# Optimization experiments

Measured on AMD Instinct MI355X. Metric: run time of the kernel, lower is better.

Reference implementation:

```python
import jax, jax.numpy as jnp
import numpy as np

N_EMBED = 1024
NUM_HEADS = 16
HEAD_SIZE = 64  # NUM_HEADS * HEAD_SIZE == N_EMBED
BLOCK_SIZE = 2048


def setup_inputs() -> dict:
    key = jax.random.key(0)
    ks = jax.random.split(key, 9)
    s = 1.0 / np.sqrt(N_EMBED)
    batch_x = jax.random.normal(ks[0], (4, BLOCK_SIZE, N_EMBED), dtype=jnp.float32)
    # stacked per-head linear params: weight [H, E, d], bias [H, d]
    Wq = jax.random.uniform(ks[1], (NUM_HEADS, N_EMBED, HEAD_SIZE), jnp.float32, -s, s)
    Wk = jax.random.uniform(ks[2], (NUM_HEADS, N_EMBED, HEAD_SIZE), jnp.float32, -s, s)
    Wv = jax.random.uniform(ks[3], (NUM_HEADS, N_EMBED, HEAD_SIZE), jnp.float32, -s, s)
    bq = jax.random.uniform(ks[4], (NUM_HEADS, HEAD_SIZE), jnp.float32, -s, s)
    bk = jax.random.uniform(ks[5], (NUM_HEADS, HEAD_SIZE), jnp.float32, -s, s)
    bv = jax.random.uniform(ks[6], (NUM_HEADS, HEAD_SIZE), jnp.float32, -s, s)
    Wp = jax.random.uniform(ks[7], (N_EMBED, N_EMBED), jnp.float32, -s, s)
    bp = jax.random.uniform(ks[8], (N_EMBED,), jnp.float32, -s, s)
    return {"batch_x": batch_x, "Wq": Wq, "Wk": Wk, "Wv": Wv,
            "bq": bq, "bk": bk, "bv": bv, "Wp": Wp, "bp": bp}


def reference(batch_x, Wq, Wk, Wv, bq, bk, bv, Wp, bp):
    B, T, E = batch_x.shape
    # per-head projections: [B, H, T, d]
    q = jnp.einsum('bte,hed->bhtd', batch_x, Wq) + bq[None, :, None, :]
    k = jnp.einsum('bte,hed->bhtd', batch_x, Wk) + bk[None, :, None, :]
    v = jnp.einsum('bte,hed->bhtd', batch_x, Wv) + bv[None, :, None, :]
    scale = 1.0 / jnp.sqrt(jnp.asarray(HEAD_SIZE, batch_x.dtype))
    wei = jnp.einsum('bhtd,bhsd->bhts', q, k) * scale  # [B,H,T,T]
    causal = jnp.tril(jnp.ones((T, T), dtype=bool))
    wei = jnp.where(causal, wei, jnp.asarray(-jnp.inf, wei.dtype))
    wei = jax.nn.softmax(wei, axis=-1)
    out = jnp.einsum('bhts,bhsd->bhtd', wei, v)  # [B,H,T,d]
    # concat heads (head order matches torch.cat over ModuleList)
    out = out.transpose(0, 2, 1, 3).reshape(B, T, NUM_HEADS * HEAD_SIZE)
    return out @ Wp + bp
```

## Files before the change

kernel.cpp:

```cpp
#include <hip/hip_runtime.h>
#include <math.h>

#define B_ 4
#define T_ 2048
#define E_ 1024
#define H_ 16
#define D_ 64

typedef __bf16 bf16_t;
typedef bf16_t bf16x8 __attribute__((ext_vector_type(8)));
typedef float  f32x4  __attribute__((ext_vector_type(4)));
typedef float  f32x16 __attribute__((ext_vector_type(16)));
typedef unsigned short u16x4 __attribute__((ext_vector_type(4)));
typedef unsigned int   u32x4 __attribute__((ext_vector_type(4)));

static __device__ __forceinline__ unsigned short f2bf(float f) {
    bf16_t h = (bf16_t)f;
    return __builtin_bit_cast(unsigned short, h);
}
static __device__ __forceinline__ unsigned int pk2(float a, float b) {
    return (unsigned int)f2bf(a) | ((unsigned int)f2bf(b) << 16);
}
static __device__ __forceinline__ float ex2(float x) {
    float r; asm("v_exp_f32 %0, %1" : "=v"(r) : "v"(x)); return r;
}
static __device__ __forceinline__ void pl32swap(unsigned int& a, unsigned int& b) {
    asm("v_permlane32_swap_b32 %0, %1" : "+v"(a), "+v"(b));
}

#define GLD(gp, lp) __builtin_amdgcn_global_load_lds( \
    (const __attribute__((address_space(1))) unsigned int*)(gp), \
    (__attribute__((address_space(3))) unsigned int*)(lp), 16, 0, 0)

#define BAR() __builtin_amdgcn_s_barrier()
#define WAIT_LGKM0() asm volatile("s_waitcnt lgkmcnt(0)" ::: "memory")
#define VMC(n) asm volatile("s_waitcnt vmcnt(" #n ")" ::: "memory")

__global__ void cast_x_kernel(const float* __restrict__ in, unsigned short* __restrict__ out, int n4) {
    int i = blockIdx.x * blockDim.x + threadIdx.x;
    if (i >= n4) return;
    float4 v = ((const float4*)in)[i];
    ushort4 o;
    o.x = f2bf(v.x); o.y = f2bf(v.y); o.z = f2bf(v.z); o.w = f2bf(v.w);
    ((ushort4*)out)[i] = o;
}

__global__ void tcast_all(const float* __restrict__ Wq, const float* __restrict__ Wk,
                          const float* __restrict__ Wv, const float* __restrict__ Wp,
                          unsigned short* __restrict__ wf, unsigned short* __restrict__ wpt) {
    __shared__ unsigned short Ts[64 * 66];
    const int grp = blockIdx.y >> 4, yy = blockIdx.y & 15;
    const float* in; unsigned short* out; int yA, S;
    if (grp == 3) { in = Wp; out = wpt; yA = 64;    S = 1024; }
    else {
        in = (grp == 0) ? Wq : (grp == 1) ? Wk : Wv;
        out = wf + (size_t)grp * 1024 * 1024; yA = 65536; S = 64;
    }
    const int tid = threadIdx.x;
    const int r = tid >> 2, c4 = tid & 3;
    const float* ip = in + (size_t)yA * yy + (size_t)(blockIdx.x * 64 + r) * S + c4 * 16;
    #pragma unroll
    for (int j = 0; j < 4; ++j) {
        float4 v = *(const float4*)&ip[j * 4];
        Ts[(c4 * 16 + j * 4 + 0) * 66 + r] = f2bf(v.x);
        Ts[(c4 * 16 + j * 4 + 1) * 66 + r] = f2bf(v.y);
        Ts[(c4 * 16 + j * 4 + 2) * 66 + r] = f2bf(v.z);
        Ts[(c4 * 16 + j * 4 + 3) * 66 + r] = f2bf(v.w);
    }
    __syncthreads();
    unsigned short* op = out + (size_t)(yy * 64 + r) * 1024 + blockIdx.x * 64 + c4 * 16;
    #pragma unroll
    for (int j = 0; j < 4; ++j) {
        u16x4 pk;
        #pragma unroll
        for (int m = 0; m < 4; ++m) pk[m] = Ts[r * 66 + c4 * 16 + j * 4 + m];
        *(u16x4*)&op[j * 4] = pk;
    }
}


#define GEMM_CORE_DECLS \
    const int tid = threadIdx.x; \
    const int w = tid >> 6, lane = tid & 63; \
    const int wr = w >> 2, wc = w & 3; \
    const int l15 = lane & 15, quad = lane >> 4, lsw = l15 & 7; \
    const int rowg = lane >> 3; \
    const int swz = ((lane & 7) ^ rowg) * 8; \
    f32x4 acc[4][4]; \
    _Pragma("unroll") for (int i_ = 0; i_ < 4; ++i_) \
        _Pragma("unroll") for (int j_ = 0; j_ < 4; ++j_) \
            acc[i_][j_] = (f32x4){0.f, 0.f, 0.f, 0.f};

#define MFMA_P(nb) \
    __builtin_amdgcn_s_setprio(1); \
    _Pragma("unroll") for (int m_ = 0; m_ < 4; ++m_) \
        _Pragma("unroll") for (int j_ = 0; j_ < 2; ++j_) \
            _Pragma("unroll") for (int k_ = 0; k_ < 2; ++k_) \
                acc[m_][(nb) + j_] = __builtin_amdgcn_mfma_f32_16x16x32_bf16( \
                    fA[m_][k_], fB[(nb) + j_][k_], acc[m_][(nb) + j_], 0, 0, 0); \
    __builtin_amdgcn_s_setprio(0);

#define GEMM_K_LOOP \
    stageA(0, 0); stageA(0, 1); stageB(0, 0, 0); stageB(0, 0, 1); \
    stageB(0, 1, 0); stageB(0, 1, 1); \
    stageA(1, 0); stageA(1, 1); stageB(1, 0, 0); stageB(1, 0, 1); \
    VMC(6); BAR(); \
    _Pragma("unroll 1") \
    for (int it = 0; it < 8; ++it) { \
        const int t0 = 2 * it, t1 = 2 * it + 1; \
        const bool more = it < 7; \
        bf16x8 fA[4][2], fB[4][2]; \
         \
        _Pragma("unroll") for (int m_ = 0; m_ < 4; ++m_) { fA[m_][0] = rdA(t0, m_, 0); fA[m_][1] = rdA(t0, m_, 1); } \
        _Pragma("unroll") for (int n_ = 0; n_ < 2; ++n_) { fB[n_][0] = rdB(t0, n_, 0); fB[n_][1] = rdB(t0, n_, 1); } \
        stageB(t1, 1, 0); stageB(t1, 1, 1); \
        BAR(); WAIT_LGKM0(); \
        MFMA_P(0); \
        VMC(6); BAR(); \
         \
        _Pragma("unroll") for (int n_ = 0; n_ < 2; ++n_) { fB[2 + n_][0] = rdB(t0, 2 + n_, 0); fB[2 + n_][1] = rdB(t0, 2 + n_, 1); } \
        if (more) { stageA(t0 + 2, 0); stageA(t0 + 2, 1); stageB(t0 + 2, 0, 0); stageB(t0 + 2, 0, 1); } \
        BAR(); WAIT_LGKM0(); \
        MFMA_P(2); \
        if (more) { VMC(6); } else { VMC(2); } \
        BAR(); \
         \
        _Pragma("unroll") for (int m_ = 0; m_ < 4; ++m_) { fA[m_][0] = rdA(t1, m_, 0); fA[m_][1] = rdA(t1, m_, 1); } \
        _Pragma("unroll") for (int n_ = 0; n_ < 2; ++n_) { fB[n_][0] = rdB(t1, n_, 0); fB[n_][1] = rdB(t1, n_, 1); } \
        if (more) { stageB(t0 + 2, 1, 0); stageB(t0 + 2, 1, 1); } \
        BAR(); WAIT_LGKM0(); \
        MFMA_P(0); \
        if (more) { VMC(6); } else { VMC(0); } \
        BAR(); \
         \
        _Pragma("unroll") for (int n_ = 0; n_ < 2; ++n_) { fB[2 + n_][0] = rdB(t1, 2 + n_, 0); fB[2 + n_][1] = rdB(t1, 2 + n_, 1); } \
        if (more) { stageA(t1 + 2, 0); stageA(t1 + 2, 1); stageB(t1 + 2, 0, 0); stageB(t1 + 2, 0, 1); } \
        BAR(); WAIT_LGKM0(); \
        MFMA_P(2); \
        if (more) { VMC(6); } \
        BAR(); \
    }

__global__ __launch_bounds__(512, 2) void qkv_gemm(
    const unsigned short* __restrict__ xb,
    const unsigned short* __restrict__ wf,
    const float* __restrict__ bq, const float* __restrict__ bk, const float* __restrict__ bv,
    unsigned short* __restrict__ qo, unsigned short* __restrict__ ko,
    unsigned short* __restrict__ vt)
{
    __shared__ __align__(16) unsigned short sm[49152];

    const int bid = blockIdx.x;
    const int m0 = (bid & 63) * 128;
    const int n0 = (bid >> 6) * 256;

    GEMM_CORE_DECLS

    auto stageA = [&](int t, int g) {
        const int rb = w * 16 + g * 8;
        unsigned short* dst = sm + (t & 1) * 24576 + rb * 64;
        GLD(xb + (size_t)(m0 + rb + rowg) * 1024 + t * 64 + swz, dst);
    };
    auto stageB = [&](int t, int R, int g) {
        const int rb = w * 16 + g * 8;
        const int ar0 = (rb >> 5) * 64 + R * 32 + (rb & 31);
        unsigned short* dst = sm + (t & 1) * 24576 + 8192 + ar0 * 64;
        GLD(wf + (size_t)(n0 + ar0 + rowg) * 1024 + t * 64 + swz, dst);
    };
    auto rdA = [&](int t, int fm, int ks) {
        const int row = wr * 64 + fm * 16 + l15;
        return *(const bf16x8*)&sm[(t & 1) * 24576 + row * 64 + (((ks * 4 + quad) ^ lsw) * 8)];
    };
    auto rdB = [&](int t, int fn, int ks) {
        const int row = wc * 64 + fn * 16 + l15;
        return *(const bf16x8*)&sm[(t & 1) * 24576 + 8192 + row * 64 + (((ks * 4 + quad) ^ lsw) * 8)];
    };

    GEMM_K_LOOP

    const int which = n0 >> 10;
    const int nb = n0 & 1023;
    if (which < 2) {
        const float* bias = which ? bk : bq;
        unsigned short* outp = which ? ko : qo;
        const float sc = which ? 1.f : 0.125f * 1.44269504088896f;
        #pragma unroll
        for (int fm = 0; fm < 4; ++fm)
            #pragma unroll
            for (int fn = 0; fn < 4; ++fn) {
                int colg = nb + wc * 64 + fn * 16 + l15;
                int h = colg >> 6, d = colg & 63;
                float bi = bias[colg];
                #pragma unroll
                for (int r = 0; r < 4; ++r) {
                    int row = m0 + wr * 64 + fm * 16 + quad * 4 + r;
                    int b = row >> 11, t = row & 2047;
                    outp[(((size_t)b * 16 + h) * 2048 + t) * 64 + d] = f2bf((acc[fm][fn][r] + bi) * sc);
                }
            }
    } else {
        const int b = m0 >> 11, t0r = m0 & 2047;
        for (int nh = 0; nh < 2; ++nh) {
            __syncthreads();
            if ((wc >> 1) == nh) {
                const int cc = wc & 1;
                #pragma unroll
                for (int fm = 0; fm < 4; ++fm)
                    #pragma unroll
                    for (int fn = 0; fn < 4; ++fn) {
                        int colL = cc * 64 + fn * 16 + l15;
                        int colg = nb + nh * 128 + colL;
                        float bi = bv[colg];
                        u16x4 pk;
                        #pragma unroll
                        for (int r = 0; r < 4; ++r) pk[r] = f2bf(acc[fm][fn][r] + bi);
                        *(u16x4*)&sm[colL * 136 + wr * 64 + fm * 16 + quad * 4] = pk;
                    }
            }
            __syncthreads();
            const int nl = tid >> 2, tq = tid & 3;
            const int colg = nb + nh * 128 + nl;
            const int h = colg >> 6, d = colg & 63;
            unsigned short* dst = vt + (((size_t)b * 16 + h) * 64 + d) * 2048 + t0r + tq * 32;
            #pragma unroll
            for (int j = 0; j < 4; ++j)
                *(float4*)&dst[j * 8] = *(const float4*)&sm[nl * 136 + tq * 32 + j * 8];
        }
    }
}

__global__ __launch_bounds__(512, 2) void proj_gemm(
    const unsigned short* __restrict__ A,
    const unsigned short* __restrict__ wpt,
    const float* __restrict__ bp,
    float* __restrict__ out)
{
    __shared__ __align__(16) unsigned short sm[49152];

    const int bid = blockIdx.x;
    const int m0 = (bid & 63) * 128;
    const int n0 = (bid >> 6) * 256;

    GEMM_CORE_DECLS

    const unsigned short* Ab = A + (size_t)(m0 >> 11) * 16 * 131072 + (size_t)(m0 & 2047) * 64;
    auto stageA = [&](int t, int g) {
        const int rb = w * 16 + g * 8;
        unsigned short* dst = sm + (t & 1) * 24576 + rb * 64;
        GLD(Ab + (size_t)t * 131072 + (rb + rowg) * 64 + swz, dst);
    };
    auto stageB = [&](int t, int R, int g) {
        const int rb = w * 16 + g * 8;
        const int ar0 = (rb >> 5) * 64 + R * 32 + (rb & 31);
        unsigned short* dst = sm + (t & 1) * 24576 + 8192 + ar0 * 64;
        GLD(wpt + (size_t)(n0 + ar0 + rowg) * 1024 + t * 64 + swz, dst);
    };
    auto rdA = [&](int t, int fm, int ks) {
        const int row = wr * 64 + fm * 16 + l15;
        return *(const bf16x8*)&sm[(t & 1) * 24576 + row * 64 + (((ks * 4 + quad) ^ lsw) * 8)];
    };
    auto rdB = [&](int t, int fn, int ks) {
        const int row = wc * 64 + fn * 16 + l15;
        return *(const bf16x8*)&sm[(t & 1) * 24576 + 8192 + row * 64 + (((ks * 4 + quad) ^ lsw) * 8)];
    };

    GEMM_K_LOOP

    #pragma unroll
    for (int fm = 0; fm < 4; ++fm)
        #pragma unroll
        for (int fn = 0; fn < 4; ++fn) {
            int col = n0 + wc * 64 + fn * 16 + l15;
            float bi = bp[col];
            #pragma unroll
            for (int r = 0; r < 4; ++r) {
                int row = m0 + wr * 64 + fm * 16 + quad * 4 + r;
                out[(size_t)row * 1024 + col] = acc[fm][fn][r] + bi;
            }
        }
}

__global__ __launch_bounds__(512, 4) void attn_kernel(
    const unsigned short* __restrict__ q, const unsigned short* __restrict__ k,
    const unsigned short* __restrict__ vt, unsigned short* __restrict__ att2)
{
    __shared__ __align__(16) unsigned short KV[2][2][8192];

    const int tid = threadIdx.x;
    const int w = tid >> 6, lane = tid & 63;
    const int l31 = lane & 31, h = lane >> 5;
    const int qg2 = w >> 1, ksel = w & 1;
    const int bh = blockIdx.x;
    const int rs = l31 & 7, rv = l31 & 15;

    const unsigned short* kb = k  + (size_t)bh * 2048 * 64;
    const unsigned short* vb = vt + (size_t)bh * 64 * 2048;

    u32x4 onesu; onesu[0] = onesu[1] = onesu[2] = onesu[3] = 0x3F803F80u;
    const bf16x8 bOnes = __builtin_bit_cast(bf16x8, onesu);

    const size_t kOff = (size_t)(16 * w + (lane >> 3)) * 64 + (size_t)(((lane & 7) ^ (lane >> 3)) * 8);
    const int vRow = lane >> 4, vc = lane & 15;
    size_t vOff[2];
    #pragma unroll
    for (int r = 0; r < 2; ++r) {
        const int drow = 8 * w + 4 * r + vRow;
        vOff[r] = (size_t)drow * 2048 + (size_t)((vc ^ (drow & 15)) * 8);
    }

    auto stage = [&](int jt, int buf) {
        unsigned short* dK = &KV[buf][0][w * 1024];
        unsigned short* dV = &KV[buf][1][w * 1024];
        const unsigned short* sK = kb + kOff + (size_t)jt * 8192;
        #pragma unroll
        for (int r = 0; r < 2; ++r) GLD(sK + r * 512, dK + r * 512);
        #pragma unroll
        for (int r = 0; r < 2; ++r) GLD(vb + vOff[r] + jt * 128, dV + r * 512);
    };

    for (int leg = 0; leg < 2; ++leg) {
        const int qtile = leg ? (15 - (int)blockIdx.y) : (int)blockIdx.y;
        const int qb0 = qtile * 128;
        const int qmin = qb0 + qg2 * 32, qmax = qmin + 31;
        const int qg = qmin + l31;
        const int trips = qtile + 1;

        bf16x8 fQ[4];
        {
            const unsigned short* qp = q + ((size_t)bh * 2048 + qg) * 64 + h * 8;
            #pragma unroll
            for (int ks = 0; ks < 4; ++ks) fQ[ks] = *(const bf16x8*)&qp[ks * 16];
        }

        f32x16 O[2], Osum;
        #pragma unroll
        for (int nt = 0; nt < 2; ++nt)
            #pragma unroll
            for (int i = 0; i < 16; ++i) O[nt][i] = 0.f;
        #pragma unroll
        for (int i = 0; i < 16; ++i) Osum[i] = 0.f;

        stage(0, 0);
        VMC(0);
        BAR();

        for (int jt = 0; jt < trips; ++jt) {
            const int buf = jt & 1;
            if (jt + 1 < trips) stage(jt + 1, buf ^ 1);
            const unsigned short* Ks = KV[buf][0];
            const unsigned short* Vs = KV[buf][1];
            const int key0 = jt * 128;

            f32x16 S[2];
            #pragma unroll
            for (int ktl = 0; ktl < 2; ++ktl)
                #pragma unroll
                for (int i = 0; i < 16; ++i) S[ktl][i] = 0.f;
            __builtin_amdgcn_s_setprio(1);
            #pragma unroll
            for (int ktl = 0; ktl < 2; ++ktl) {
                const int ktg = 2 * ksel + ktl;
                if (key0 + 32 * ktg <= qmax) {
                    const int row = ktg * 32 + l31;
                    #pragma unroll
                    for (int ks = 0; ks < 4; ++ks) {
                        bf16x8 aK = *(const bf16x8*)&Ks[row * 64 + (((2 * ks + h) ^ rs) * 8)];
                        S[ktl] = __builtin_amdgcn_mfma_f32_32x32x16_bf16(aK, fQ[ks], S[ktl], 0, 0, 0);
                    }
                }
            }
            __builtin_amdgcn_s_setprio(0);

            #pragma unroll
            for (int ktl = 0; ktl < 2; ++ktl) {
                const int ktg = 2 * ksel + ktl;
                if (key0 + 32 * ktg <= qmax) {
                    const bool nm = (key0 + 32 * ktg + 31) > qmin;
                    unsigned int e0[4], e1[4];
                    #pragma unroll
                    for (int g = 0; g < 4; ++g) {
                        float p[4];
                        #pragma unroll
                        for (int r = 0; r < 4; ++r) {
                            float pv = ex2(S[ktl][4 * g + r]);
                            if (nm) {
                                int key = key0 + ktg * 32 + 8 * g + 4 * h + r;
                                if (key > qg) pv = 0.f;
                            }
                            p[r] = pv;
                        }
                        e0[g] = pk2(p[0], p[1]);
                        e1[g] = pk2(p[2], p[3]);
                    }

                    __builtin_amdgcn_s_setprio(1);
                    #pragma unroll
                    for (int s = 0; s < 2; ++s) {
                        unsigned int a = e0[2 * s], b = e0[2 * s + 1];
                        pl32swap(a, b);
                        unsigned int c2 = e1[2 * s], d2 = e1[2 * s + 1];
                        pl32swap(c2, d2);
                        u32x4 t; t[0] = a; t[1] = c2; t[2] = b; t[3] = d2;
                        bf16x8 aP = __builtin_bit_cast(bf16x8, t);
                        const int cb = 4 * ktg + 2 * s;
                        #pragma unroll
                        for (int nt = 0; nt < 2; ++nt) {
                            const int drow = nt * 32 + l31;
                            bf16x8 bV = *(const bf16x8*)&Vs[drow * 128 + (((cb + h) ^ rv) * 8)];
                            O[nt] = __builtin_amdgcn_mfma_f32_32x32x16_bf16(aP, bV, O[nt], 0, 0, 0);
                        }
                        Osum = __builtin_amdgcn_mfma_f32_32x32x16_bf16(aP, bOnes, Osum, 0, 0, 0);
                    }
                    __builtin_amdgcn_s_setprio(0);
                }
            }

            VMC(0);
            BAR();
        }

        float* Lf = (float*)KV;
        __syncthreads();
        float* mb = Lf + (size_t)qg2 * 48 * 64;
        if (ksel) {
            #pragma unroll
            for (int nt = 0; nt < 2; ++nt)
                #pragma unroll
                for (int i = 0; i < 16; ++i)
                    mb[(nt * 16 + i) * 64 + lane] = O[nt][i];
            #pragma unroll
            for (int i = 0; i < 16; ++i)
                mb[(32 + i) * 64 + lane] = Osum[i];
        }
        __syncthreads();
        if (!ksel) {
            #pragma unroll
            for (int nt = 0; nt < 2; ++nt)
                #pragma unroll
                for (int i = 0; i < 16; ++i)
                    O[nt][i] += mb[(nt * 16 + i) * 64 + lane];
            #pragma unroll
            for (int i = 0; i < 16; ++i)
                Osum[i] += mb[(32 + i) * 64 + lane];

            unsigned short* ob = att2 + ((size_t)bh * 2048 + qmin) * 64;
            #pragma unroll
            for (int g = 0; g < 4; ++g)
                #pragma unroll
                for (int r = 0; r < 4; ++r) {
                    const float iv = 1.f / Osum[4 * g + r];
                    const int qy = 8 * g + 4 * h + r;
                    #pragma unroll
                    for (int nt = 0; nt < 2; ++nt)
                        ob[(size_t)qy * 64 + nt * 32 + l31] = f2bf(O[nt][4 * g + r] * iv);
                }
        }
        __syncthreads();
    }
}

extern "C" void kernel_launch(void* const* d_in, const int* in_sizes, int n_in,
                              void* d_out, int out_size, void* d_ws, size_t ws_size,
                              hipStream_t stream) {
    const float* x  = (const float*)d_in[0];
    const float* Wq = (const float*)d_in[1];
    const float* Wk = (const float*)d_in[2];
    const float* Wv = (const float*)d_in[3];
    const float* bq = (const float*)d_in[4];
    const float* bk = (const float*)d_in[5];
    const float* bv = (const float*)d_in[6];
    const float* Wp = (const float*)d_in[7];
    const float* bp = (const float*)d_in[8];
    float* out = (float*)d_out;

    const size_t nx = (size_t)B_ * T_ * E_;
    unsigned short* base = (unsigned short*)d_ws;
    unsigned short* xb  = base;
    unsigned short* qb  = xb + nx;
    unsigned short* kb  = qb + nx;
    unsigned short* vtb = kb + nx;
    unsigned short* atb = vtb + nx;
    unsigned short* wf  = atb + nx;
    unsigned short* wpt = wf + 3072 * 1024;

    cast_x_kernel<<<(int)(nx / 4 + 255) / 256, 256, 0, stream>>>(x, xb, (int)(nx / 4));
    tcast_all<<<dim3(16, 64), 256, 0, stream>>>(Wq, Wk, Wv, Wp, wf, wpt);
    qkv_gemm<<<768, 512, 0, stream>>>(xb, wf, bq, bk, bv, qb, kb, vtb);
    attn_kernel<<<dim3(64, 8), 512, 0, stream>>>(qb, kb, vtb, atb);
    proj_gemm<<<256, 512, 0, stream>>>(atb, wpt, bp, out);
}
```

Before: 255.1 us.

## Halve attention KV tile to 64 keys and merge cast kernels

The attention kernel now stages 64-key K/V tiles instead of 128, which halves LDS use per block and raises the launch-bounds occupancy target from 4 to 8 blocks. Each wave handles one 32-key subtile per trip, so the trip count doubles. The cross-wave reduction at the end is split into two halves to fit the smaller shared buffer. The x-cast and weight-transpose kernels are merged into one launch to save a kernel launch, at the cost of more barriers and loop iterations per tile and tighter register limits.

```diff
diff --git a/kernel.cpp b/kernel.cpp
--- a/kernel.cpp
+++ b/kernel.cpp
@@ -36,29 +36,32 @@
 #define WAIT_LGKM0() asm volatile("s_waitcnt lgkmcnt(0)" ::: "memory")
 #define VMC(n) asm volatile("s_waitcnt vmcnt(" #n ")" ::: "memory")
 
-__global__ void cast_x_kernel(const float* __restrict__ in, unsigned short* __restrict__ out, int n4) {
-    int i = blockIdx.x * blockDim.x + threadIdx.x;
-    if (i >= n4) return;
-    float4 v = ((const float4*)in)[i];
-    ushort4 o;
-    o.x = f2bf(v.x); o.y = f2bf(v.y); o.z = f2bf(v.z); o.w = f2bf(v.w);
-    ((ushort4*)out)[i] = o;
-}
-
-__global__ void tcast_all(const float* __restrict__ Wq, const float* __restrict__ Wk,
-                          const float* __restrict__ Wv, const float* __restrict__ Wp,
-                          unsigned short* __restrict__ wf, unsigned short* __restrict__ wpt) {
+__global__ void prep_kernel(const float* __restrict__ xin, unsigned short* __restrict__ xb,
+                            const float* __restrict__ Wq, const float* __restrict__ Wk,
+                            const float* __restrict__ Wv, const float* __restrict__ Wp,
+                            unsigned short* __restrict__ wf, unsigned short* __restrict__ wpt) {
     __shared__ unsigned short Ts[64 * 66];
-    const int grp = blockIdx.y >> 4, yy = blockIdx.y & 15;
+    const int bid = blockIdx.x;
+    const int tid = threadIdx.x;
+    if (bid < 8192) {
+        int i = bid * 256 + tid;
+        float4 v = ((const float4*)xin)[i];
+        ushort4 o;
+        o.x = f2bf(v.x); o.y = f2bf(v.y); o.z = f2bf(v.z); o.w = f2bf(v.w);
+        ((ushort4*)xb)[i] = o;
+        return;
+    }
+    const int b2 = bid - 8192;
+    const int bx = b2 & 15, by = b2 >> 4;
+    const int grp = by >> 4, yy = by & 15;
     const float* in; unsigned short* out; int yA, S;
     if (grp == 3) { in = Wp; out = wpt; yA = 64;    S = 1024; }
     else {
         in = (grp == 0) ? Wq : (grp == 1) ? Wk : Wv;
         out = wf + (size_t)grp * 1024 * 1024; yA = 65536; S = 64;
     }
-    const int tid = threadIdx.x;
     const int r = tid >> 2, c4 = tid & 3;
-    const float* ip = in + (size_t)yA * yy + (size_t)(blockIdx.x * 64 + r) * S + c4 * 16;
+    const float* ip = in + (size_t)yA * yy + (size_t)(bx * 64 + r) * S + c4 * 16;
     #pragma unroll
     for (int j = 0; j < 4; ++j) {
         float4 v = *(const float4*)&ip[j * 4];
@@ -68,7 +71,7 @@
         Ts[(c4 * 16 + j * 4 + 3) * 66 + r] = f2bf(v.w);
     }
     __syncthreads();
-    unsigned short* op = out + (size_t)(yy * 64 + r) * 1024 + blockIdx.x * 64 + c4 * 16;
+    unsigned short* op = out + (size_t)(yy * 64 + r) * 1024 + bx * 64 + c4 * 16;
     #pragma unroll
     for (int j = 0; j < 4; ++j) {
         u16x4 pk;
@@ -280,18 +283,18 @@
         }
 }
 
-__global__ __launch_bounds__(512, 4) void attn_kernel(
+__global__ __launch_bounds__(512, 8) void attn_kernel(
     const unsigned short* __restrict__ q, const unsigned short* __restrict__ k,
     const unsigned short* __restrict__ vt, unsigned short* __restrict__ att2)
 {
-    __shared__ __align__(16) unsigned short KV[2][2][8192];
+    __shared__ __align__(16) unsigned short KV[2][2][4096];
 
     const int tid = threadIdx.x;
     const int w = tid >> 6, lane = tid & 63;
     const int l31 = lane & 31, h = lane >> 5;
     const int qg2 = w >> 1, ksel = w & 1;
     const int bh = blockIdx.x;
-    const int rs = l31 & 7, rv = l31 & 15;
+    const int rs = l31 & 7;
 
     const unsigned short* kb = k  + (size_t)bh * 2048 * 64;
     const unsigned short* vb = vt + (size_t)bh * 64 * 2048;
@@ -299,23 +302,13 @@
     u32x4 onesu; onesu[0] = onesu[1] = onesu[2] = onesu[3] = 0x3F803F80u;
     const bf16x8 bOnes = __builtin_bit_cast(bf16x8, onesu);
 
-    const size_t kOff = (size_t)(16 * w + (lane >> 3)) * 64 + (size_t)(((lane & 7) ^ (lane >> 3)) * 8);
-    const int vRow = lane >> 4, vc = lane & 15;
-    size_t vOff[2];
-    #pragma unroll
-    for (int r = 0; r < 2; ++r) {
-        const int drow = 8 * w + 4 * r + vRow;
-        vOff[r] = (size_t)drow * 2048 + (size_t)((vc ^ (drow & 15)) * 8);
-    }
+    const int rg = lane >> 3;
+    const size_t kOff = (size_t)(8 * w + rg) * 64 + (size_t)(((lane & 7) ^ rg) * 8);
+    const size_t vOff = (size_t)(8 * w + rg) * 2048 + (size_t)(((lane & 7) ^ rg) * 8);
 
     auto stage = [&](int jt, int buf) {
-        unsigned short* dK = &KV[buf][0][w * 1024];
-        unsigned short* dV = &KV[buf][1][w * 1024];
-        const unsigned short* sK = kb + kOff + (size_t)jt * 8192;
-        #pragma unroll
-        for (int r = 0; r < 2; ++r) GLD(sK + r * 512, dK + r * 512);
-        #pragma unroll
-        for (int r = 0; r < 2; ++r) GLD(vb + vOff[r] + jt * 128, dV + r * 512);
+        GLD(kb + kOff + (size_t)jt * 4096, &KV[buf][0][w * 512]);
+        GLD(vb + vOff + jt * 64,           &KV[buf][1][w * 512]);
     };
 
     for (int leg = 0; leg < 2; ++leg) {
@@ -323,7 +316,7 @@
         const int qb0 = qtile * 128;
         const int qmin = qb0 + qg2 * 32, qmax = qmin + 31;
         const int qg = qmin + l31;
-        const int trips = qtile + 1;
+        const int trips = 2 * qtile + 2;
 
         bf16x8 fQ[4];
         {
@@ -349,70 +342,60 @@
             if (jt + 1 < trips) stage(jt + 1, buf ^ 1);
             const unsigned short* Ks = KV[buf][0];
             const unsigned short* Vs = KV[buf][1];
-            const int key0 = jt * 128;
-
-            f32x16 S[2];
-            #pragma unroll
-            for (int ktl = 0; ktl < 2; ++ktl)
-                #pragma unroll
-                for (int i = 0; i < 16; ++i) S[ktl][i] = 0.f;
-            __builtin_amdgcn_s_setprio(1);
-            #pragma unroll
-            for (int ktl = 0; ktl < 2; ++ktl) {
-                const int ktg = 2 * ksel + ktl;
-                if (key0 + 32 * ktg <= qmax) {
-                    const int row = ktg * 32 + l31;
+            const int wk0 = jt * 64 + 32 * ksel;
+
+            if (wk0 <= qmax) {
+                f32x16 S;
+                #pragma unroll
+                for (int i = 0; i < 16; ++i) S[i] = 0.f;
+                __builtin_amdgcn_s_setprio(1);
+                {
+                    const int row = 32 * ksel + l31;
                     #pragma unroll
                     for (int ks = 0; ks < 4; ++ks) {
                         bf16x8 aK = *(const bf16x8*)&Ks[row * 64 + (((2 * ks + h) ^ rs) * 8)];
-                        S[ktl] = __builtin_amdgcn_mfma_f32_32x32x16_bf16(aK, fQ[ks], S[ktl], 0, 0, 0);
+                        S = __builtin_amdgcn_mfma_f32_32x32x16_bf16(aK, fQ[ks], S, 0, 0, 0);
                     }
                 }
-            }
-            __builtin_amdgcn_s_setprio(0);
-
-            #pragma unroll
-            for (int ktl = 0; ktl < 2; ++ktl) {
-                const int ktg = 2 * ksel + ktl;
-                if (key0 + 32 * ktg <= qmax) {
-                    const bool nm = (key0 + 32 * ktg + 31) > qmin;
-                    unsigned int e0[4], e1[4];
-                    #pragma unroll
-                    for (int g = 0; g < 4; ++g) {
-                        float p[4];
-                        #pragma unroll
-                        for (int r = 0; r < 4; ++r) {
-                            float pv = ex2(S[ktl][4 * g + r]);
-                            if (nm) {
-                                int key = key0 + ktg * 32 + 8 * g + 4 * h + r;
-                                if (key > qg) pv = 0.f;
-                            }
-                            p[r] = pv;
+                __builtin_amdgcn_s_setprio(0);
+
+                const bool nm = (wk0 + 31) > qmin;
+                unsigned int e0[4], e1[4];
+                #pragma unroll
+                for (int g = 0; g < 4; ++g) {
+                    float p[4];
+                    #pragma unroll
+                    for (int r = 0; r < 4; ++r) {
+                        float pv = ex2(S[4 * g + r]);
+                        if (nm) {
+                            int key = wk0 + 8 * g + 4 * h + r;
+                            if (key > qg) pv = 0.f;
                         }
-                        e0[g] = pk2(p[0], p[1]);
-                        e1[g] = pk2(p[2], p[3]);
+                        p[r] = pv;
                     }
-
-                    __builtin_amdgcn_s_setprio(1);
-                    #pragma unroll
-                    for (int s = 0; s < 2; ++s) {
-                        unsigned int a = e0[2 * s], b = e0[2 * s + 1];
-                        pl32swap(a, b);
-                        unsigned int c2 = e1[2 * s], d2 = e1[2 * s + 1];
-                        pl32swap(c2, d2);
-                        u32x4 t; t[0] = a; t[1] = c2; t[2] = b; t[3] = d2;
-                        bf16x8 aP = __builtin_bit_cast(bf16x8, t);
-                        const int cb = 4 * ktg + 2 * s;
-                        #pragma unroll
-                        for (int nt = 0; nt < 2; ++nt) {
-                            const int drow = nt * 32 + l31;
-                            bf16x8 bV = *(const bf16x8*)&Vs[drow * 128 + (((cb + h) ^ rv) * 8)];
-                            O[nt] = __builtin_amdgcn_mfma_f32_32x32x16_bf16(aP, bV, O[nt], 0, 0, 0);
-                        }
-                        Osum = __builtin_amdgcn_mfma_f32_32x32x16_bf16(aP, bOnes, Osum, 0, 0, 0);
+                    e0[g] = pk2(p[0], p[1]);
+                    e1[g] = pk2(p[2], p[3]);
+                }
+
+                __builtin_amdgcn_s_setprio(1);
+                #pragma unroll
+                for (int s = 0; s < 2; ++s) {
+                    unsigned int a = e0[2 * s], b = e0[2 * s + 1];
+                    pl32swap(a, b);
+                    unsigned int c2 = e1[2 * s], d2 = e1[2 * s + 1];
+                    pl32swap(c2, d2);
+                    u32x4 t; t[0] = a; t[1] = c2; t[2] = b; t[3] = d2;
+                    bf16x8 aP = __builtin_bit_cast(bf16x8, t);
+                    const int cb = 4 * ksel + 2 * s;
+                    #pragma unroll
+                    for (int nt = 0; nt < 2; ++nt) {
+                        const int drow = nt * 32 + l31;
+                        bf16x8 bV = *(const bf16x8*)&Vs[drow * 64 + (((cb + h) ^ rs) * 8)];
+                        O[nt] = __builtin_amdgcn_mfma_f32_32x32x16_bf16(aP, bV, O[nt], 0, 0, 0);
                     }
-                    __builtin_amdgcn_s_setprio(0);
+                    Osum = __builtin_amdgcn_mfma_f32_32x32x16_bf16(aP, bOnes, Osum, 0, 0, 0);
                 }
+                __builtin_amdgcn_s_setprio(0);
             }
 
             VMC(0);
@@ -420,40 +403,42 @@
         }
 
         float* Lf = (float*)KV;
-        __syncthreads();
-        float* mb = Lf + (size_t)qg2 * 48 * 64;
-        if (ksel) {
-            #pragma unroll
-            for (int nt = 0; nt < 2; ++nt)
+        for (int half = 0; half < 2; ++half) {
+            __syncthreads();
+            float* mb = Lf + (size_t)(qg2 & 1) * 48 * 64;
+            if ((qg2 >> 1) == half && ksel) {
+                #pragma unroll
+                for (int nt = 0; nt < 2; ++nt)
+                    #pragma unroll
+                    for (int i = 0; i < 16; ++i)
+                        mb[(nt * 16 + i) * 64 + lane] = O[nt][i];
                 #pragma unroll
                 for (int i = 0; i < 16; ++i)
-                    mb[(nt * 16 + i) * 64 + lane] = O[nt][i];
-            #pragma unroll
-            for (int i = 0; i < 16; ++i)
-                mb[(32 + i) * 64 + lane] = Osum[i];
-        }
-        __syncthreads();
-        if (!ksel) {
-            #pragma unroll
-            for (int nt = 0; nt < 2; ++nt)
+                    mb[(32 + i) * 64 + lane] = Osum[i];
+            }
+            __syncthreads();
+            if ((qg2 >> 1) == half && !ksel) {
+                #pragma unroll
+                for (int nt = 0; nt < 2; ++nt)
+                    #pragma unroll
+                    for (int i = 0; i < 16; ++i)
+                        O[nt][i] += mb[(nt * 16 + i) * 64 + lane];
                 #pragma unroll
                 for (int i = 0; i < 16; ++i)
-                    O[nt][i] += mb[(nt * 16 + i) * 64 + lane];
-            #pragma unroll
-            for (int i = 0; i < 16; ++i)
-                Osum[i] += mb[(32 + i) * 64 + lane];
-
-            unsigned short* ob = att2 + ((size_t)bh * 2048 + qmin) * 64;
-            #pragma unroll
-            for (int g = 0; g < 4; ++g)
-                #pragma unroll
-                for (int r = 0; r < 4; ++r) {
-                    const float iv = 1.f / Osum[4 * g + r];
-                    const int qy = 8 * g + 4 * h + r;
-                    #pragma unroll
-                    for (int nt = 0; nt < 2; ++nt)
-                        ob[(size_t)qy * 64 + nt * 32 + l31] = f2bf(O[nt][4 * g + r] * iv);
-                }
+                    Osum[i] += mb[(32 + i) * 64 + lane];
+
+                unsigned short* ob = att2 + ((size_t)bh * 2048 + qmin) * 64;
+                #pragma unroll
+                for (int g = 0; g < 4; ++g)
+                    #pragma unroll
+                    for (int r = 0; r < 4; ++r) {
+                        const float iv = 1.f / Osum[4 * g + r];
+                        const int qy = 8 * g + 4 * h + r;
+                        #pragma unroll
+                        for (int nt = 0; nt < 2; ++nt)
+                            ob[(size_t)qy * 64 + nt * 32 + l31] = f2bf(O[nt][4 * g + r] * iv);
+                    }
+            }
         }
         __syncthreads();
     }
@@ -483,8 +468,7 @@
     unsigned short* wf  = atb + nx;
     unsigned short* wpt = wf + 3072 * 1024;
 
-    cast_x_kernel<<<(int)(nx / 4 + 255) / 256, 256, 0, stream>>>(x, xb, (int)(nx / 4));
-    tcast_all<<<dim3(16, 64), 256, 0, stream>>>(Wq, Wk, Wv, Wp, wf, wpt);
+    prep_kernel<<<9216, 256, 0, stream>>>(x, xb, Wq, Wk, Wv, Wp, wf, wpt);
     qkv_gemm<<<768, 512, 0, stream>>>(xb, wf, bq, bk, bv, qb, kb, vtb);
     attn_kernel<<<dim3(64, 8), 512, 0, stream>>>(qb, kb, vtb, atb);
     proj_gemm<<<256, 512, 0, stream>>>(atb, wpt, bp, out);
```

Result: slower. 948.1 us (+271.7%).
